# Kernel optimization log

Measured on AMD Instinct MI355X. Metric: run time of the kernel, lower is better.

Reference implementation:

```python
import jax, jax.numpy as jnp
import numpy as np

N_NODES = 40000
N_EDGES = 640000
NUM_GRAPHS = 64
NODE_DIM = 128
EDGE_DIM = 32
HID = 64
AGG_HID = 128
NEG_SLOPE = 0.2


def _segment_softmax(logits, seg, num_segments):
    # logits: [E, H], seg: [E] target-node index. Numerically stable per-segment softmax.
    m = jax.ops.segment_max(logits, seg, num_segments=num_segments)
    m = jnp.where(jnp.isfinite(m), m, 0.0)  # empty segments -> -inf max
    e = jnp.exp(logits - m[seg])
    denom = jax.ops.segment_sum(e, seg, num_segments=num_segments)
    return e / (denom[seg] + 1e-16)


def gatv2_conv(x, edge_index, edge_attr, Wl, bl, Wr, br, We, att, bias, concat):
    # PyG GATv2Conv with edge features (share_weights=False, lin_edge bias-free).
    N = x.shape[0]
    H, C = att.shape
    src, dst = edge_index[0], edge_index[1]
    xl = (x @ Wl + bl).reshape(N, H, C)          # lin_l(x) -> source transform
    xr = (x @ Wr + br).reshape(N, H, C)          # lin_r(x) -> target transform
    ee = (edge_attr @ We).reshape(-1, H, C)       # lin_edge(edge_attr)
    m = jax.nn.leaky_relu(xl[src] + xr[dst] + ee, NEG_SLOPE)  # [E,H,C]
    logits = jnp.einsum('ehc,hc->eh', m, att)     # [E,H]
    alpha = _segment_softmax(logits, dst, N)      # softmax over incoming edges
    out = jax.ops.segment_sum(xl[src] * alpha[..., None], dst, num_segments=N)  # [N,H,C]
    out = out.reshape(N, H * C) if concat else out.mean(axis=1)
    return out + bias


def setup_inputs() -> dict:
    key = jax.random.key(0)
    ks = iter(jax.random.split(key, 40))
    rn = lambda shape, s=0.1: (jax.random.normal(next(ks), shape, dtype=jnp.float32) * s)
    inp = {}
    inp['x'] = jax.random.normal(next(ks), (N_NODES, NODE_DIM), dtype=jnp.float32)
    inp['edge_attr'] = jax.random.normal(next(ks), (N_EDGES, EDGE_DIM), dtype=jnp.float32)
    inp['edge_index'] = jax.random.randint(next(ks), (2, N_EDGES), 0, N_NODES, dtype=jnp.int32)
    inp['batch'] = jnp.sort(jax.random.randint(next(ks), (N_NODES,), 0, NUM_GRAPHS, dtype=jnp.int32))
    inp.update(W1l=rn((NODE_DIM, 2 * HID)), b1l=jnp.zeros((2 * HID,), jnp.float32),
               W1r=rn((NODE_DIM, 2 * HID)), b1r=jnp.zeros((2 * HID,), jnp.float32),
               W1e=rn((EDGE_DIM, 2 * HID)), att1=rn((2, HID)), bias1=jnp.zeros((2 * HID,), jnp.float32))
    inp.update(W2l=rn((2 * HID, 2 * HID)), b2l=jnp.zeros((2 * HID,), jnp.float32),
               W2r=rn((2 * HID, 2 * HID)), b2r=jnp.zeros((2 * HID,), jnp.float32),
               W2e=rn((EDGE_DIM, 2 * HID)), att2=rn((2, HID)), bias2=jnp.zeros((2 * HID,), jnp.float32))
    # conv3: 128 -> 64, 1 head, concat=False
    inp.update(W3l=rn((2 * HID, HID)), b3l=jnp.zeros((HID,), jnp.float32),
               W3r=rn((2 * HID, HID)), b3r=jnp.zeros((HID,), jnp.float32),
               W3e=rn((EDGE_DIM, HID)), att3=rn((1, HID)), bias3=jnp.zeros((HID,), jnp.float32))
    inp.update(G1w=rn((HID, AGG_HID)), G1b=jnp.zeros((AGG_HID,), jnp.float32),
               G2w=rn((AGG_HID, 1)), G2b=jnp.zeros((1,), jnp.float32),
               Wreg=rn((HID, 1)), breg=jnp.zeros((1,), jnp.float32))
    return inp


def reference(x, edge_attr, edge_index, batch,
              W1l, b1l, W1r, b1r, W1e, att1, bias1,
              W2l, b2l, W2r, b2r, W2e, att2, bias2,
              W3l, b3l, W3r, b3r, W3e, att3, bias3,
              G1w, G1b, G2w, G2b, Wreg, breg):
    h = jax.nn.relu(gatv2_conv(x, edge_index, edge_attr, W1l, b1l, W1r, b1r, W1e, att1, bias1, True))
    h = jax.nn.relu(gatv2_conv(h, edge_index, edge_attr, W2l, b2l, W2r, b2r, W2e, att2, bias2, True))
    h = gatv2_conv(h, edge_index, edge_attr, W3l, b3l, W3r, b3r, W3e, att3, bias3, False)  # [N, HID]
    # Attentional aggregation over nodes, per graph
    gate = (jax.nn.relu(h @ G1w + G1b) @ G2w + G2b)[:, 0]            # [N]
    gate = _segment_softmax(gate[:, None], batch, NUM_GRAPHS)[:, 0]   # softmax within each graph
    pooled = jax.ops.segment_sum(gate[:, None] * h, batch, num_segments=NUM_GRAPHS)  # [B, HID]
    return (pooled @ Wreg + breg).squeeze(-1)  # [B]
```

## Files before the change

### kernel.cpp

```cpp
#include <hip/hip_runtime.h>

__global__ void k_fill(unsigned* p, int n, unsigned v) {
    int i = blockIdx.x * blockDim.x + threadIdx.x;
    if (i < n) p[i] = v;
}

__global__ void k_hist(const int* __restrict__ ei, int E, int* __restrict__ deg) {
    int e = blockIdx.x * blockDim.x + threadIdx.x;
    if (e < E) atomicAdd(&deg[ei[E + e]], 1);
}

__global__ void k_scan_blocks(const int* __restrict__ deg, int N,
                              int* __restrict__ excl, int* __restrict__ parts) {
    __shared__ int s[256];
    int t = threadIdx.x, i = blockIdx.x * 256 + t;
    int v = (i < N) ? deg[i] : 0;
    s[t] = v;
    __syncthreads();
    int acc = v;
    for (int off = 1; off < 256; off <<= 1) {
        int add = (t >= off) ? s[t - off] : 0;
        __syncthreads();
        acc += add;
        s[t] = acc;
        __syncthreads();
    }
    if (i < N) excl[i] = acc - v;
    if (t == 255) parts[blockIdx.x] = acc;
}

__global__ void k_scan_parts(int* __restrict__ parts, int nb) {
    __shared__ int s[256];
    int t = threadIdx.x;
    int v = (t < nb) ? parts[t] : 0;
    s[t] = v;
    __syncthreads();
    int acc = v;
    for (int off = 1; off < 256; off <<= 1) {
        int add = (t >= off) ? s[t - off] : 0;
        __syncthreads();
        acc += add;
        s[t] = acc;
        __syncthreads();
    }
    if (t < nb) parts[t] = acc - v;
}

__global__ void k_scan_add(const int* __restrict__ excl, const int* __restrict__ parts,
                           int* __restrict__ row_ptr, int* __restrict__ cursor, int N) {
    int i = blockIdx.x * blockDim.x + threadIdx.x;
    if (i >= N) return;
    int r = excl[i] + parts[i >> 8];
    row_ptr[i] = r;
    cursor[i] = r;
}

__global__ void k_scatter(const int* __restrict__ ei, int E, int* __restrict__ cursor,
                          int2* __restrict__ elist) {
    int e = blockIdx.x * blockDim.x + threadIdx.x;
    if (e >= E) return;
    int d = ei[E + e];
    int j = atomicAdd(&cursor[d], 1);
    elist[j] = make_int2(ei[e], e);
}

__global__ void k_reorder(const int2* __restrict__ elist, const float* __restrict__ ea, int E,
                          float4* __restrict__ ea_s) {
    int idx = blockIdx.x * blockDim.x + threadIdx.x;
    int j = idx >> 3, q = idx & 7;
    if (j >= E) return;
    ea_s[(size_t)j * 8 + q] = ((const float4*)ea)[(size_t)elist[j].y * 8 + q];
}

template <int M, int RW>
__global__ __launch_bounds__(256) void k_gemm2(const float* __restrict__ A,
                                               const float* __restrict__ Wl, const float* __restrict__ bl,
                                               const float* __restrict__ Wr, const float* __restrict__ br,
                                               float* __restrict__ outl, float* __restrict__ outr) {
    constexpr int TX = M / 4;
    __shared__ float sA[32][68];
    __shared__ float sW[32][M];
    const float* W    = blockIdx.y ? Wr : Wl;
    const float* bias = blockIdx.y ? br : bl;
    float* out        = blockIdx.y ? outr : outl;
    int t = threadIdx.x;
    int tx = t % TX, ty = t / TX;
    int r0 = blockIdx.x * 64;
    float acc[RW][4] = {};
    for (int kt = 0; kt < 128; kt += 32) {
        for (int l = t; l < 512; l += 256) {
            int row = l >> 3, kq = (l & 7) << 2;
            float4 a = *(const float4*)&A[(size_t)(r0 + row) * 128 + kt + kq];
            sA[kq + 0][row] = a.x; sA[kq + 1][row] = a.y;
            sA[kq + 2][row] = a.z; sA[kq + 3][row] = a.w;
        }
        for (int l = t; l < 32 * M / 4; l += 256) {
            int kk = (l * 4) / M, cc = (l * 4) % M;
            *(float4*)&sW[kk][cc] = *(const float4*)&W[(size_t)(kt + kk) * M + cc];
        }
        __syncthreads();
#pragma unroll
        for (int k = 0; k < 32; k++) {
            float4 w = *(float4*)&sW[k][tx * 4];
            float ar[RW];
#pragma unroll
            for (int i = 0; i < RW; i += 4) {
                float4 a = *(float4*)&sA[k][ty * RW + i];
                ar[i] = a.x; ar[i + 1] = a.y; ar[i + 2] = a.z; ar[i + 3] = a.w;
            }
#pragma unroll
            for (int i = 0; i < RW; i++) {
                acc[i][0] += ar[i] * w.x; acc[i][1] += ar[i] * w.y;
                acc[i][2] += ar[i] * w.z; acc[i][3] += ar[i] * w.w;
            }
        }
        __syncthreads();
    }
    float4 b = *(const float4*)&bias[tx * 4];
#pragma unroll
    for (int i = 0; i < RW; i++) {
        float4 v;
        v.x = acc[i][0] + b.x; v.y = acc[i][1] + b.y;
        v.z = acc[i][2] + b.z; v.w = acc[i][3] + b.w;
        *(float4*)&out[(size_t)(r0 + ty * RW + i) * M + tx * 4] = v;
    }
}

template <int H, bool RELU, bool SORTED>
__global__ __launch_bounds__(256) void k_agg(const float* __restrict__ xl, const float* __restrict__ xr,
                                             const float* __restrict__ ea, const float4* __restrict__ ea_s,
                                             const int2* __restrict__ elist,
                                             const int* __restrict__ row_ptr, const int* __restrict__ deg,
                                             const float* __restrict__ We, const float* __restrict__ att,
                                             const float* __restrict__ bias, float* __restrict__ out, int N) {
    constexpr int HC = H * 64;
    int tid = threadIdx.x, wv = tid >> 6, lane = tid & 63;
    float rWe0[32], rWe1[H == 2 ? 32 : 1];
#pragma unroll
    for (int k = 0; k < 32; k++) rWe0[k] = We[k * HC + lane];
    if constexpr (H == 2) {
#pragma unroll
        for (int k = 0; k < 32; k++) rWe1[k] = We[k * HC + 64 + lane];
    }
    float att0 = att[lane], b0 = bias[lane];
    float att1 = 0.f, b1 = 0.f;
    if constexpr (H == 2) { att1 = att[64 + lane]; b1 = bias[64 + lane]; }
    int n = blockIdx.x * 4 + wv;
    if (n >= N) return;
    int start = row_ptr[n], d = deg[n];
    float xr0 = xr[(size_t)n * HC + lane];
    float xr1 = (H == 2) ? xr[(size_t)n * HC + 64 + lane] : 0.f;
    float acc0 = 0.f, acc1 = 0.f, den0 = 0.f, den1 = 0.f;
    for (int j = 0; j < d; j++) {
        int2 sp = elist[start + j];
        const float4* eap = SORTED ? (ea_s + (size_t)(start + j) * 8)
                                   : (const float4*)(ea + (size_t)sp.y * 32);
        const float* xls = xl + (size_t)sp.x * HC;
        float xl0 = xls[lane];
        float xl1 = (H == 2) ? xls[64 + lane] : 0.f;
        float ee0 = 0.f, ee1 = 0.f;
#pragma unroll
        for (int kq = 0; kq < 8; kq++) {
            float4 v = eap[kq];
            ee0 = fmaf(v.x, rWe0[kq * 4 + 0], ee0);
            ee0 = fmaf(v.y, rWe0[kq * 4 + 1], ee0);
            ee0 = fmaf(v.z, rWe0[kq * 4 + 2], ee0);
            ee0 = fmaf(v.w, rWe0[kq * 4 + 3], ee0);
            if constexpr (H == 2) {
                ee1 = fmaf(v.x, rWe1[kq * 4 + 0], ee1);
                ee1 = fmaf(v.y, rWe1[kq * 4 + 1], ee1);
                ee1 = fmaf(v.z, rWe1[kq * 4 + 2], ee1);
                ee1 = fmaf(v.w, rWe1[kq * 4 + 3], ee1);
            }
        }
        float v0 = xl0 + xr0 + ee0;
        v0 = v0 > 0.f ? v0 : 0.2f * v0;
        float p0 = att0 * v0, p1 = 0.f;
        if constexpr (H == 2) {
            float v1 = xl1 + xr1 + ee1;
            v1 = v1 > 0.f ? v1 : 0.2f * v1;
            p1 = att1 * v1;
        }
#pragma unroll
        for (int m = 32; m; m >>= 1) {
            p0 += __shfl_xor(p0, m);
            if constexpr (H == 2) p1 += __shfl_xor(p1, m);
        }
        float ex0 = __expf(p0);
        acc0 = fmaf(ex0, xl0, acc0);
        den0 += ex0;
        if constexpr (H == 2) {
            float ex1 = __expf(p1);
            acc1 = fmaf(ex1, xl1, acc1);
            den1 += ex1;
        }
    }
    float o0 = acc0 / (den0 + 1e-16f) + b0;
    if (RELU) o0 = o0 > 0.f ? o0 : 0.f;
    out[(size_t)n * HC + lane] = o0;
    if constexpr (H == 2) {
        float o1 = acc1 / (den1 + 1e-16f) + b1;
        if (RELU) o1 = o1 > 0.f ? o1 : 0.f;
        out[(size_t)n * HC + 64 + lane] = o1;
    }
}

__global__ __launch_bounds__(256) void k_gate(const float* __restrict__ h, const float* __restrict__ G1w,
                                              const float* __restrict__ G1b, const float* __restrict__ G2w,
                                              const float* __restrict__ G2b,
                                              float* __restrict__ gate, int N) {
    __shared__ float sH[64][64];
    __shared__ float part[64][2];
    int t = threadIdx.x;
    int n0 = blockIdx.x * 64;
    for (int l = t; l < 1024; l += 256) {
        float4 v = ((const float4*)(h + (size_t)n0 * 64))[l];
        int n = l >> 4, kq = (l & 15) << 2;
        *(float4*)&sH[n][kq] = v;
    }
    int c = t & 127, half = t >> 7;
    float rW[64];
#pragma unroll
    for (int k = 0; k < 64; k++) rW[k] = G1w[k * 128 + c];
    float g1b = G1b[c], g2w = G2w[c];
    __syncthreads();
    for (int nn = 0; nn < 32; nn++) {
        int n = half * 32 + nn;
        float acc = g1b;
#pragma unroll
        for (int k = 0; k < 64; k += 4) {
            float4 hv = *(const float4*)&sH[n][k];
            acc = fmaf(hv.x, rW[k], acc);
            acc = fmaf(hv.y, rW[k + 1], acc);
            acc = fmaf(hv.z, rW[k + 2], acc);
            acc = fmaf(hv.w, rW[k + 3], acc);
        }
        acc = acc > 0.f ? acc : 0.f;
        float p = acc * g2w;
#pragma unroll
        for (int m = 32; m; m >>= 1) p += __shfl_xor(p, m);
        if ((t & 63) == 0) part[n][(t >> 6) & 1] = p;
    }
    __syncthreads();
    if (t < 64) gate[n0 + t] = __expf(part[t][0] + part[t][1] + G2b[0]);
}

__global__ __launch_bounds__(256) void k_pool(const float* __restrict__ h, const float* __restrict__ gate,
                                              const int* __restrict__ batch,
                                              float* __restrict__ pooled, int N) {
    int g = blockIdx.x;
    int lo = 0, hi = N;
    while (lo < hi) { int mid = (lo + hi) >> 1; if (batch[mid] < g) lo = mid + 1; else hi = mid; }
    int start = lo;
    lo = 0; hi = N;
    while (lo < hi) { int mid = (lo + hi) >> 1; if (batch[mid] < g + 1) lo = mid + 1; else hi = mid; }
    int end = lo;
    int t = threadIdx.x, wv = t >> 6, lane = t & 63;
    float acc = 0.f, den = 0.f;
    for (int n = start + wv; n < end; n += 4) {
        float gv = gate[n];
        acc = fmaf(gv, h[(size_t)n * 64 + lane], acc);
        den += gv;
    }
    __shared__ float sacc[4][64];
    __shared__ float sden[4];
    sacc[wv][lane] = acc;
    if (lane == 0) sden[wv] = den;
    __syncthreads();
    if (wv == 0) {
        float a = sacc[0][lane] + sacc[1][lane] + sacc[2][lane] + sacc[3][lane];
        float d = sden[0] + sden[1] + sden[2] + sden[3] + 1e-16f;
        pooled[g * 64 + lane] = a / d;
    }
}

__global__ void k_final(const float* __restrict__ pooled, const float* __restrict__ Wreg,
                        const float* __restrict__ breg, float* __restrict__ out) {
    int g = threadIdx.x;
    float acc = breg[0];
    for (int c = 0; c < 64; c++) acc += pooled[g * 64 + c] * Wreg[c];
    out[g] = acc;
}

extern "C" void kernel_launch(void* const* d_in, const int* in_sizes, int n_in,
                              void* d_out, int out_size, void* d_ws, size_t ws_size,
                              hipStream_t stream) {
    const float* x  = (const float*)d_in[0];
    const float* ea = (const float*)d_in[1];
    const int* ei    = (const int*)d_in[2];
    const int* batch = (const int*)d_in[3];
    auto ff = [&](int i) { return (const float*)d_in[i]; };
    const float *W1l = ff(4), *b1l = ff(5), *W1r = ff(6), *b1r = ff(7), *W1e = ff(8),
                *att1 = ff(9), *bias1 = ff(10);
    const float *W2l = ff(11), *b2l = ff(12), *W2r = ff(13), *b2r = ff(14), *W2e = ff(15),
                *att2 = ff(16), *bias2 = ff(17);
    const float *W3l = ff(18), *b3l = ff(19), *W3r = ff(20), *b3r = ff(21), *W3e = ff(22),
                *att3 = ff(23), *bias3 = ff(24);
    const float *G1w = ff(25), *G1b = ff(26), *G2w = ff(27), *G2b = ff(28), *Wreg = ff(29),
                *breg = ff(30);

    const int N = in_sizes[0] / 128;
    const int E = in_sizes[2] / 2;

    char* ws = (char*)d_ws;
    float*  bufA    = (float*)(ws);
    float*  bufB    = (float*)(ws + 20480000);
    float*  bufH    = (float*)(ws + 40960000);
    int2*   elist   = (int2*)(ws + 61440000);
    int*    row_ptr = (int*)(ws + 66560000);
    int*    deg     = (int*)(ws + 66720000);
    int*    cursor  = (int*)(ws + 66880000);
    int*    excl    = (int*)(ws + 67040000);
    int*    parts   = (int*)(ws + 67200000);
    float*  gate    = (float*)(ws + 67204096);
    float*  pooled  = (float*)(ws + 67364096);
    float4* ea_s    = (float4*)(ws + 67380480);
    const bool sorted_ea = ws_size >= (size_t)67380480 + (size_t)E * 32 * 4;

    auto cdiv = [](int a, int b) { return (a + b - 1) / b; };
    const int NB = cdiv(N, 256);
    const dim3 gemmG(N / 64, 2);
    const int AGGB = cdiv(N, 4);

    k_fill<<<NB, 256, 0, stream>>>((unsigned*)deg, N, 0u);
    k_hist<<<cdiv(E, 256), 256, 0, stream>>>(ei, E, deg);
    k_scan_blocks<<<NB, 256, 0, stream>>>(deg, N, excl, parts);
    k_scan_parts<<<1, 256, 0, stream>>>(parts, NB);
    k_scan_add<<<NB, 256, 0, stream>>>(excl, parts, row_ptr, cursor, N);
    k_scatter<<<cdiv(E, 256), 256, 0, stream>>>(ei, E, cursor, elist);
    if (sorted_ea)
        k_reorder<<<cdiv(E * 8, 256), 256, 0, stream>>>(elist, ea, E, ea_s);

    k_gemm2<128, 8><<<gemmG, 256, 0, stream>>>(x, W1l, b1l, W1r, b1r, bufA, bufB);
    if (sorted_ea)
        k_agg<2, true, true><<<AGGB, 256, 0, stream>>>(bufA, bufB, ea, ea_s, elist, row_ptr, deg, W1e, att1, bias1, bufH, N);
    else
        k_agg<2, true, false><<<AGGB, 256, 0, stream>>>(bufA, bufB, ea, ea_s, elist, row_ptr, deg, W1e, att1, bias1, bufH, N);

    k_gemm2<128, 8><<<gemmG, 256, 0, stream>>>(bufH, W2l, b2l, W2r, b2r, bufA, bufB);
    if (sorted_ea)
        k_agg<2, true, true><<<AGGB, 256, 0, stream>>>(bufA, bufB, ea, ea_s, elist, row_ptr, deg, W2e, att2, bias2, bufH, N);
    else
        k_agg<2, true, false><<<AGGB, 256, 0, stream>>>(bufA, bufB, ea, ea_s, elist, row_ptr, deg, W2e, att2, bias2, bufH, N);

    k_gemm2<64, 4><<<gemmG, 256, 0, stream>>>(bufH, W3l, b3l, W3r, b3r, bufA, bufB);
    if (sorted_ea)
        k_agg<1, false, true><<<AGGB, 256, 0, stream>>>(bufA, bufB, ea, ea_s, elist, row_ptr, deg, W3e, att3, bias3, bufH, N);
    else
        k_agg<1, false, false><<<AGGB, 256, 0, stream>>>(bufA, bufB, ea, ea_s, elist, row_ptr, deg, W3e, att3, bias3, bufH, N);

    k_gate<<<N / 64, 256, 0, stream>>>(bufH, G1w, G1b, G2w, G2b, gate, N);
    k_pool<<<64, 256, 0, stream>>>(bufH, gate, batch, pooled, N);
    k_final<<<1, 64, 0, stream>>>(pooled, Wreg, breg, (float*)d_out);
}
```

Measured before the change: 1.065 ms.

## Split GATv2 aggregation into edge-parallel logit GEMM and node-parallel softmax-sum

Each layer's per-node aggregation is replaced by two kernels. An edge-parallel kernel computes the edge-feature projection as a shared-memory tiled GEMM over 64-edge tiles, fuses the leaky-ReLU and attention dot product, and writes per-edge logits. A node-parallel kernel then sums exp(logit)·xl over incoming edges, with two waves per node and prefetching of the next edge. It also drops the sorted edge-attribute copy in favour of split src/eid arrays plus a dst array, and skips the softmax max subtraction, which risks overflow if logits grow large.

New measurement: 1.738 ms. 1.63x slower.

```diff
diff --git a/kernel.cpp b/kernel.cpp
--- a/kernel.cpp
+++ b/kernel.cpp
@@ -56,20 +56,21 @@
 }
 
 __global__ void k_scatter(const int* __restrict__ ei, int E, int* __restrict__ cursor,
-                          int2* __restrict__ elist) {
+                          int* __restrict__ esrc, int* __restrict__ eeid) {
     int e = blockIdx.x * blockDim.x + threadIdx.x;
     if (e >= E) return;
     int d = ei[E + e];
     int j = atomicAdd(&cursor[d], 1);
-    elist[j] = make_int2(ei[e], e);
-}
-
-__global__ void k_reorder(const int2* __restrict__ elist, const float* __restrict__ ea, int E,
-                          float4* __restrict__ ea_s) {
-    int idx = blockIdx.x * blockDim.x + threadIdx.x;
-    int j = idx >> 3, q = idx & 7;
-    if (j >= E) return;
-    ea_s[(size_t)j * 8 + q] = ((const float4*)ea)[(size_t)elist[j].y * 8 + q];
+    esrc[j] = ei[e];
+    eeid[j] = e;
+}
+
+__global__ void k_dstfill(const int* __restrict__ row_ptr, const int* __restrict__ deg,
+                          int* __restrict__ edst, int N) {
+    int n = blockIdx.x * blockDim.x + threadIdx.x;
+    if (n >= N) return;
+    int s = row_ptr[n], d = deg[n];
+    for (int i = 0; i < d; i++) edst[s + i] = n;
 }
 
 template <int M, int RW>
@@ -126,13 +127,154 @@
     }
 }
 
-template <int H, bool RELU, bool SORTED>
-__global__ __launch_bounds__(256) void k_agg(const float* __restrict__ xl, const float* __restrict__ xr,
-                                             const float* __restrict__ ea, const float4* __restrict__ ea_s,
-                                             const int2* __restrict__ elist,
-                                             const int* __restrict__ row_ptr, const int* __restrict__ deg,
-                                             const float* __restrict__ We, const float* __restrict__ att,
-                                             const float* __restrict__ bias, float* __restrict__ out, int N) {
+template <int HC>
+__global__ __launch_bounds__(256) void k_elogit(const float* __restrict__ ea,
+                                                const int* __restrict__ eeid,
+                                                const int* __restrict__ esrc,
+                                                const int* __restrict__ edst,
+                                                const float* __restrict__ We,
+                                                const float* __restrict__ att,
+                                                const float* __restrict__ xl,
+                                                const float* __restrict__ xr,
+                                                float* __restrict__ logit, int E) {
+    constexpr int ROWS = 64;
+    constexpr int TX = HC / 4;
+    constexpr int RW = ROWS / (256 / TX);
+    __shared__ float sA[32][ROWS + 4];
+    __shared__ float sW[32][HC];
+    int sb = blockIdx.x * ROWS;
+    if (sb >= E) return;
+    int t = threadIdx.x;
+    for (int l = t; l < ROWS * 8; l += 256) {
+        int row = l >> 3, kq = (l & 7) << 2;
+        int s = sb + row;
+        int eid = (s < E) ? eeid[s] : 0;
+        float4 a = *(const float4*)&ea[(size_t)eid * 32 + kq];
+        sA[kq + 0][row] = a.x; sA[kq + 1][row] = a.y;
+        sA[kq + 2][row] = a.z; sA[kq + 3][row] = a.w;
+    }
+    for (int l = t; l < 32 * HC / 4; l += 256) {
+        int k = (l * 4) / HC, c = (l * 4) % HC;
+        *(float4*)&sW[k][c] = *(const float4*)&We[k * HC + c];
+    }
+    __syncthreads();
+    int tx = t % TX, ty = t / TX;
+    float4 attv = *(const float4*)&att[tx * 4];
+    float acc[RW][4] = {};
+#pragma unroll
+    for (int k = 0; k < 32; k++) {
+        float4 w = *(float4*)&sW[k][tx * 4];
+        float ar[RW];
+#pragma unroll
+        for (int i = 0; i < RW; i += 4) {
+            float4 a = *(float4*)&sA[k][ty * RW + i];
+            ar[i] = a.x; ar[i + 1] = a.y; ar[i + 2] = a.z; ar[i + 3] = a.w;
+        }
+#pragma unroll
+        for (int i = 0; i < RW; i++) {
+            acc[i][0] = fmaf(ar[i], w.x, acc[i][0]);
+            acc[i][1] = fmaf(ar[i], w.y, acc[i][1]);
+            acc[i][2] = fmaf(ar[i], w.z, acc[i][2]);
+            acc[i][3] = fmaf(ar[i], w.w, acc[i][3]);
+        }
+    }
+#pragma unroll
+    for (int i = 0; i < RW; i++) {
+        int s = sb + ty * RW + i;
+        bool ok = s < E;
+        int src = ok ? esrc[s] : 0;
+        int dst = ok ? edst[s] : 0;
+        float4 xl4 = *(const float4*)&xl[(size_t)src * HC + tx * 4];
+        float4 xr4 = *(const float4*)&xr[(size_t)dst * HC + tx * 4];
+        float v0 = acc[i][0] + xl4.x + xr4.x; v0 = v0 > 0.f ? v0 : 0.2f * v0;
+        float v1 = acc[i][1] + xl4.y + xr4.y; v1 = v1 > 0.f ? v1 : 0.2f * v1;
+        float v2 = acc[i][2] + xl4.z + xr4.z; v2 = v2 > 0.f ? v2 : 0.2f * v2;
+        float v3 = acc[i][3] + xl4.w + xr4.w; v3 = v3 > 0.f ? v3 : 0.2f * v3;
+        float p = fmaf(attv.x, v0, fmaf(attv.y, v1, fmaf(attv.z, v2, attv.w * v3)));
+#pragma unroll
+        for (int m = 1; m < 16; m <<= 1) p += __shfl_xor(p, m);
+        if constexpr (HC == 128) {
+            if ((tx & 15) == 0 && ok) logit[2 * (size_t)s + (tx >> 4)] = p;
+        } else {
+            if (tx == 0 && ok) logit[s] = p;
+        }
+    }
+}
+
+template <int H, bool RELU>
+__global__ __launch_bounds__(256) void k_aggv(const float* __restrict__ xl,
+                                              const float* __restrict__ logit,
+                                              const int* __restrict__ esrc,
+                                              const int* __restrict__ row_ptr, const int* __restrict__ deg,
+                                              const float* __restrict__ bias,
+                                              float* __restrict__ out, int N) {
+    constexpr int HC = H * 64;
+    __shared__ float2 sAcc[2][64];
+    __shared__ float  sDen[2][64];
+    int tid = threadIdx.x, wv = tid >> 6, lane = tid & 63;
+    int ns = wv >> 1, eh = wv & 1;
+    int n = blockIdx.x * 2 + ns;
+    bool alive = n < N;
+    int hf = lane >> 5, c2 = lane & 31;
+    int col = (H == 2) ? (hf * 64 + 2 * c2) : (2 * c2);
+    int start = 0, d = 0;
+    if (alive) { start = row_ptr[n]; d = deg[n]; }
+    float2 acc = make_float2(0.f, 0.f);
+    float den = 0.f;
+    const int jstep = (H == 2) ? 2 : 4;
+    int jc = (H == 2) ? eh : (2 * eh + hf);
+
+    bool okc = jc < d;
+    int sC = start + jc, sN = sC + jstep;
+    float lgC = 0.f;
+    float2 xlC = make_float2(0.f, 0.f);
+    if (okc) {
+        lgC = (H == 2) ? logit[2 * (size_t)sC + hf] : logit[sC];
+        xlC = *(const float2*)&xl[(size_t)esrc[sC] * HC + col];
+    }
+    bool okn = (jc + jstep) < d;
+    while (okc) {
+        float lgN = 0.f;
+        float2 xlN = make_float2(0.f, 0.f);
+        if (okn) {
+            lgN = (H == 2) ? logit[2 * (size_t)sN + hf] : logit[sN];
+            xlN = *(const float2*)&xl[(size_t)esrc[sN] * HC + col];
+        }
+        float ex = __expf(lgC);
+        acc.x = fmaf(ex, xlC.x, acc.x);
+        acc.y = fmaf(ex, xlC.y, acc.y);
+        den += ex;
+        jc += jstep; sC = sN; sN += jstep;
+        lgC = lgN; xlC = xlN;
+        okc = okn; okn = (jc + jstep) < d;
+    }
+
+    if constexpr (H == 1) {
+        acc.x += __shfl_xor(acc.x, 32);
+        acc.y += __shfl_xor(acc.y, 32);
+        den   += __shfl_xor(den, 32);
+    }
+    if (eh == 1) { sAcc[ns][lane] = acc; sDen[ns][lane] = den; }
+    __syncthreads();
+    if (eh == 0 && alive) {
+        float2 a2 = sAcc[ns][lane];
+        float dsum = den + sDen[ns][lane] + 1e-16f;
+        float2 bv = *(const float2*)&bias[col];
+        float o0 = (acc.x + a2.x) / dsum + bv.x;
+        float o1 = (acc.y + a2.y) / dsum + bv.y;
+        if (RELU) { o0 = fmaxf(o0, 0.f); o1 = fmaxf(o1, 0.f); }
+        if (H == 2 || hf == 0)
+            *(float2*)&out[(size_t)n * HC + col] = make_float2(o0, o1);
+    }
+}
+
+template <int H, bool RELU>
+__global__ __launch_bounds__(256) void k_agg_fb(const float* __restrict__ xl, const float* __restrict__ xr,
+                                                const float* __restrict__ ea,
+                                                const int* __restrict__ esrc, const int* __restrict__ eeid,
+                                                const int* __restrict__ row_ptr, const int* __restrict__ deg,
+                                                const float* __restrict__ We, const float* __restrict__ att,
+                                                const float* __restrict__ bias, float* __restrict__ out, int N) {
     constexpr int HC = H * 64;
     int tid = threadIdx.x, wv = tid >> 6, lane = tid & 63;
     float rWe0[32], rWe1[H == 2 ? 32 : 1];
@@ -152,10 +294,9 @@
     float xr1 = (H == 2) ? xr[(size_t)n * HC + 64 + lane] : 0.f;
     float acc0 = 0.f, acc1 = 0.f, den0 = 0.f, den1 = 0.f;
     for (int j = 0; j < d; j++) {
-        int2 sp = elist[start + j];
-        const float4* eap = SORTED ? (ea_s + (size_t)(start + j) * 8)
-                                   : (const float4*)(ea + (size_t)sp.y * 32);
-        const float* xls = xl + (size_t)sp.x * HC;
+        int src = esrc[start + j], eid = eeid[start + j];
+        const float4* eap = (const float4*)(ea + (size_t)eid * 32);
+        const float* xls = xl + (size_t)src * HC;
         float xl0 = xls[lane];
         float xl1 = (H == 2) ? xls[64 + lane] : 0.f;
         float ee0 = 0.f, ee1 = 0.f;
@@ -306,7 +447,8 @@
     float*  bufA    = (float*)(ws);
     float*  bufB    = (float*)(ws + 20480000);
     float*  bufH    = (float*)(ws + 40960000);
-    int2*   elist   = (int2*)(ws + 61440000);
+    int*    esrc    = (int*)(ws + 61440000);
+    int*    eeid    = (int*)(ws + 64000000);
     int*    row_ptr = (int*)(ws + 66560000);
     int*    deg     = (int*)(ws + 66720000);
     int*    cursor  = (int*)(ws + 66880000);
@@ -314,40 +456,43 @@
     int*    parts   = (int*)(ws + 67200000);
     float*  gate    = (float*)(ws + 67204096);
     float*  pooled  = (float*)(ws + 67364096);
-    float4* ea_s    = (float4*)(ws + 67380480);
-    const bool sorted_ea = ws_size >= (size_t)67380480 + (size_t)E * 32 * 4;
+    int*    edst    = (int*)(ws + 67380480);
+    float*  logit   = (float*)(ws + 69940480);
+    const bool newpath = ws_size >= (size_t)69940480 + (size_t)E * 2 * 4;
 
     auto cdiv = [](int a, int b) { return (a + b - 1) / b; };
     const int NB = cdiv(N, 256);
     const dim3 gemmG(N / 64, 2);
-    const int AGGB = cdiv(N, 4);
+    const int ELB = cdiv(E, 64);
+    const int AGB = cdiv(N, 2);
 
     k_fill<<<NB, 256, 0, stream>>>((unsigned*)deg, N, 0u);
     k_hist<<<cdiv(E, 256), 256, 0, stream>>>(ei, E, deg);
     k_scan_blocks<<<NB, 256, 0, stream>>>(deg, N, excl, parts);
     k_scan_parts<<<1, 256, 0, stream>>>(parts, NB);
     k_scan_add<<<NB, 256, 0, stream>>>(excl, parts, row_ptr, cursor, N);
-    k_scatter<<<cdiv(E, 256), 256, 0, stream>>>(ei, E, cursor, elist);
-    if (sorted_ea)
-        k_reorder<<<cdiv(E * 8, 256), 256, 0, stream>>>(elist, ea, E, ea_s);
-
-    k_gemm2<128, 8><<<gemmG, 256, 0, stream>>>(x, W1l, b1l, W1r, b1r, bufA, bufB);
-    if (sorted_ea)
-        k_agg<2, true, true><<<AGGB, 256, 0, stream>>>(bufA, bufB, ea, ea_s, elist, row_ptr, deg, W1e, att1, bias1, bufH, N);
-    else
-        k_agg<2, true, false><<<AGGB, 256, 0, stream>>>(bufA, bufB, ea, ea_s, elist, row_ptr, deg, W1e, att1, bias1, bufH, N);
-
-    k_gemm2<128, 8><<<gemmG, 256, 0, stream>>>(bufH, W2l, b2l, W2r, b2r, bufA, bufB);
-    if (sorted_ea)
-        k_agg<2, true, true><<<AGGB, 256, 0, stream>>>(bufA, bufB, ea, ea_s, elist, row_ptr, deg, W2e, att2, bias2, bufH, N);
-    else
-        k_agg<2, true, false><<<AGGB, 256, 0, stream>>>(bufA, bufB, ea, ea_s, elist, row_ptr, deg, W2e, att2, bias2, bufH, N);
-
-    k_gemm2<64, 4><<<gemmG, 256, 0, stream>>>(bufH, W3l, b3l, W3r, b3r, bufA, bufB);
-    if (sorted_ea)
-        k_agg<1, false, true><<<AGGB, 256, 0, stream>>>(bufA, bufB, ea, ea_s, elist, row_ptr, deg, W3e, att3, bias3, bufH, N);
-    else
-        k_agg<1, false, false><<<AGGB, 256, 0, stream>>>(bufA, bufB, ea, ea_s, elist, row_ptr, deg, W3e, att3, bias3, bufH, N);
+    k_scatter<<<cdiv(E, 256), 256, 0, stream>>>(ei, E, cursor, esrc, eeid);
+
+    if (newpath) {
+        k_dstfill<<<NB, 256, 0, stream>>>(row_ptr, deg, edst, N);
+        k_gemm2<128, 8><<<gemmG, 256, 0, stream>>>(x, W1l, b1l, W1r, b1r, bufA, bufB);
+        k_elogit<128><<<ELB, 256, 0, stream>>>(ea, eeid, esrc, edst, W1e, att1, bufA, bufB, logit, E);
+        k_aggv<2, true><<<AGB, 256, 0, stream>>>(bufA, logit, esrc, row_ptr, deg, bias1, bufH, N);
+        k_gemm2<128, 8><<<gemmG, 256, 0, stream>>>(bufH, W2l, b2l, W2r, b2r, bufA, bufB);
+        k_elogit<128><<<ELB, 256, 0, stream>>>(ea, eeid, esrc, edst, W2e, att2, bufA, bufB, logit, E);
+        k_aggv<2, true><<<AGB, 256, 0, stream>>>(bufA, logit, esrc, row_ptr, deg, bias2, bufH, N);
+        k_gemm2<64, 4><<<gemmG, 256, 0, stream>>>(bufH, W3l, b3l, W3r, b3r, bufA, bufB);
+        k_elogit<64><<<ELB, 256, 0, stream>>>(ea, eeid, esrc, edst, W3e, att3, bufA, bufB, logit, E);
+        k_aggv<1, false><<<AGB, 256, 0, stream>>>(bufA, logit, esrc, row_ptr, deg, bias3, bufH, N);
+    } else {
+        const int AGGB = cdiv(N, 4);
+        k_gemm2<128, 8><<<gemmG, 256, 0, stream>>>(x, W1l, b1l, W1r, b1r, bufA, bufB);
+        k_agg_fb<2, true><<<AGGB, 256, 0, stream>>>(bufA, bufB, ea, esrc, eeid, row_ptr, deg, W1e, att1, bias1, bufH, N);
+        k_gemm2<128, 8><<<gemmG, 256, 0, stream>>>(bufH, W2l, b2l, W2r, b2r, bufA, bufB);
+        k_agg_fb<2, true><<<AGGB, 256, 0, stream>>>(bufA, bufB, ea, esrc, eeid, row_ptr, deg, W2e, att2, bias2, bufH, N);
+        k_gemm2<64, 4><<<gemmG, 256, 0, stream>>>(bufH, W3l, b3l, W3r, b3r, bufA, bufB);
+        k_agg_fb<1, false><<<AGGB, 256, 0, stream>>>(bufA, bufB, ea, esrc, eeid, row_ptr, deg, W3e, att3, bias3, bufH, N);
+    }
 
     k_gate<<<N / 64, 256, 0, stream>>>(bufH, G1w, G1b, G2w, G2b, gate, N);
     k_pool<<<64, 256, 0, stream>>>(bufH, gate, batch, pooled, N);
```
